# Kernel tuning notes

Measured on AMD Instinct MI355X. Metric: run time of the kernel, lower is better.

Reference implementation:

```python
import jax, jax.numpy as jnp
import numpy as np

N = 100000
E = 1600000
F_IN = 128
HID = 128
CLS = 40


def setup_inputs() -> dict:
    key = jax.random.key(0)
    ks = jax.random.split(key, 8)
    x = jax.random.normal(ks[0], (N, F_IN), dtype=jnp.float32)
    edge_index = jax.random.randint(ks[1], (2, E), 0, N, dtype=jnp.int64)
    s1 = 1.0 / np.sqrt(F_IN)
    s2 = 1.0 / np.sqrt(HID)
    return {
        "x": x,
        "edge_index": edge_index,
        "Wl1": jax.random.uniform(ks[2], (F_IN, HID), jnp.float32, -s1, s1),
        "Wr1": jax.random.uniform(ks[3], (F_IN, HID), jnp.float32, -s1, s1),
        "b1": jnp.zeros((HID,), jnp.float32),
        "Wl2": jax.random.uniform(ks[4], (HID, CLS), jnp.float32, -s2, s2),
        "Wr2": jax.random.uniform(ks[5], (HID, CLS), jnp.float32, -s2, s2),
        "b2": jnp.zeros((CLS,), jnp.float32),
    }


def _sage_conv(x, src, dst, Wl, Wr, b):
    # mean aggregation of neighbor features: messages flow src -> dst
    msg = x[src]                                                  # [E, F]
    agg = jax.ops.segment_sum(msg, dst, num_segments=N)          # [N, F]
    deg = jax.ops.segment_sum(jnp.ones((src.shape[0],), x.dtype), dst,
                              num_segments=N)                     # [N]
    mean = agg / jnp.maximum(deg, 1.0)[:, None]
    # PyG SAGEConv: lin_l(aggregated) + lin_r(root); bias on lin_l only
    return mean @ Wl + x @ Wr + b


def reference(x, edge_index, Wl1, Wr1, b1, Wl2, Wr2, b2):
    src, dst = edge_index[0], edge_index[1]
    h = _sage_conv(x, src, dst, Wl1, Wr1, b1)
    h = jax.nn.relu(h)
    # dropout is identity in eval mode
    out = _sage_conv(h, src, dst, Wl2, Wr2, b2)
    return out
```

## Files before the change

kernel.cpp:

```cpp
#include <hip/hip_runtime.h>

#define F 128
#define CLSN 40
#define NFINE_MAX 256
#define PCAP 10240
#define TILE 4096
#define STAGE_CAP 10240
#define QSCALE 22.0f

typedef __attribute__((ext_vector_type(8))) short short8v;
typedef __attribute__((ext_vector_type(4))) float float4v;

static __device__ inline ushort f2bf(float f) {
  uint u = __float_as_uint(f);
  uint r = (u + 0x7FFFu + ((u >> 16) & 1u)) >> 16;
  return (ushort)r;
}
static __device__ inline float bfLo(uint u) { return __uint_as_float(u << 16); }
static __device__ inline float bfHi(uint u) { return __uint_as_float(u & 0xFFFF0000u); }
static __device__ inline int sb(uint v, int sh) { return (int)(signed char)(v >> sh); }
static __device__ inline unsigned char q8(float f) {
  float t = rintf(f * QSCALE);
  t = fminf(fmaxf(t, -127.f), 127.f);
  return (unsigned char)(signed char)(int)t;
}
static __device__ inline unsigned char q8s(float f, float qs) {
  float t = rintf(f * qs);
  t = fminf(fmaxf(t, -127.f), 127.f);
  return (unsigned char)(signed char)(int)t;
}

__global__ __launch_bounds__(256) void k_prep(const float* __restrict__ x,
                                              ushort* __restrict__ xb,
                                              unsigned char* __restrict__ xq,
                                              const float* __restrict__ Wl1,
                                              const float* __restrict__ Wr1,
                                              ushort* __restrict__ Wp1,
                                              const float* __restrict__ Wl2,
                                              const float* __restrict__ Wr2,
                                              ushort* __restrict__ Wpl,
                                              ushort* __restrict__ Wpr,
                                              int* __restrict__ fcur,
                                              int nelem4, int castBlocks, int nfine) {
  const int blk = blockIdx.x;
  if (blk < castBlocks) {
    int i = blk * 256 + threadIdx.x;
    if (i < nelem4) {
      float4 v = reinterpret_cast<const float4*>(x)[i];
      ushort4 o;
      o.x = f2bf(v.x); o.y = f2bf(v.y); o.z = f2bf(v.z); o.w = f2bf(v.w);
      reinterpret_cast<ushort4*>(xb)[i] = o;
      uchar4 q;
      q.x = q8(v.x); q.y = q8(v.y); q.z = q8(v.z); q.w = q8(v.w);
      reinterpret_cast<uchar4*>(xq)[i] = q;
    }
  } else if (blk < castBlocks + 16) {
    int t = (blk - castBlocks) * 256 + threadIdx.x;
    int lane = t & 63, f = (t >> 6) & 7, ks = t >> 9;
    int col = f * 16 + (lane & 15);
    int k0 = ks * 32 + (lane >> 4) * 8;
#pragma unroll
    for (int j = 0; j < 8; ++j) {
      int k = k0 + j;
      float w = (k < 128) ? Wl1[k * 128 + col] : Wr1[(k - 128) * 128 + col];
      Wp1[t * 8 + j] = f2bf(w);
    }
  } else if (blk < castBlocks + 22) {
    int t = (blk - castBlocks - 16) * 256 + threadIdx.x;
    const float* W = (t < 768) ? Wl2 : Wr2;
    ushort* Wp = (t < 768) ? Wpl : Wpr;
    int tt = (t < 768) ? t : t - 768;
    int lane = tt & 63, rem = tt >> 6;
    int f = rem % 3, ks = rem / 3;
    int col = f * 16 + (lane & 15);
    int k0 = ks * 32 + (lane >> 4) * 8;
#pragma unroll
    for (int j = 0; j < 8; ++j) {
      int k = k0 + j;
      float w = (col < CLSN) ? W[k * CLSN + col] : 0.f;
      Wp[tt * 8 + j] = f2bf(w);
    }
  } else {
    int i = threadIdx.x;
    if (i < nfine) fcur[i] = i * PCAP;
  }
}

__global__ __launch_bounds__(256) void k_partition(const int* __restrict__ src,
                                                   const int* __restrict__ dst,
                                                   int* __restrict__ fcur,
                                                   uint* __restrict__ pairs, int E) {
  __shared__ int hh[NFINE_MAX];
  __shared__ int bb[NFINE_MAX];
  __shared__ unsigned char ebkt[TILE];
  __shared__ ushort dlow[TILE];
  const int tid = threadIdx.x;
  const int tile0 = blockIdx.x * TILE;
  const int lim = min(TILE, E - tile0);
  for (int i = tid; i < NFINE_MAX; i += 256) hh[i] = 0;
  __syncthreads();
  for (int i = tid; i < lim; i += 256) {
    int d = dst[tile0 + i];
    int b = d >> 9;
    ebkt[i] = (unsigned char)b;
    dlow[i] = (ushort)(d & 511);
    atomicAdd(&hh[b], 1);
  }
  __syncthreads();
  for (int i = tid; i < NFINE_MAX; i += 256) {
    int c = hh[i];
    bb[i] = c ? atomicAdd(&fcur[i], c) : 0;
    hh[i] = 0;
  }
  __syncthreads();
  for (int i = tid; i < lim; i += 256) {
    int b = ebkt[i];
    int r = atomicAdd(&hh[b], 1);
    uint p = (uint)src[tile0 + i] | ((uint)dlow[i] << 17);
    pairs[bb[b] + r] = p;
  }
}

__global__ __launch_bounds__(256) void k_local_scatter(const uint* __restrict__ pairs,
                                                       const int* __restrict__ fcur,
                                                       int* __restrict__ offsets,
                                                       int* __restrict__ srcs,
                                                       int n, int E, int nfine) {
  __shared__ int s_cnt[512];
  __shared__ int s_scan[512];
  __shared__ int s_stage[STAGE_CAP];
  const int b = blockIdx.x, tid = threadIdx.x;
  const int node0 = b << 9;
  const int pbase = b * PCAP;
  int c_i = (tid < nfine) ? (fcur[tid] - tid * PCAP) : 0;
  s_scan[tid] = c_i;
  __syncthreads();
  for (int d = 1; d < 256; d <<= 1) {
    int u = (tid >= d) ? s_scan[tid - d] : 0;
    __syncthreads();
    s_scan[tid] += u;
    __syncthreads();
  }
  const int ecnt = fcur[b] - pbase;
  const int ebase = s_scan[b] - ecnt;
  __syncthreads();
  s_cnt[tid] = 0;
  s_cnt[tid + 256] = 0;
  __syncthreads();
  for (int i = tid; i < ecnt; i += 256) atomicAdd(&s_cnt[pairs[pbase + i] >> 17], 1);
  __syncthreads();
  s_scan[tid] = s_cnt[tid];
  s_scan[tid + 256] = s_cnt[tid + 256];
  __syncthreads();
  for (int d = 1; d < 512; d <<= 1) {
    int v0 = (tid >= d) ? s_scan[tid - d] : 0;
    int v1 = (tid + 256 >= d) ? s_scan[tid + 256 - d] : 0;
    __syncthreads();
    s_scan[tid] += v0;
    s_scan[tid + 256] += v1;
    __syncthreads();
  }
  int e0 = s_scan[tid] - s_cnt[tid];
  int e1 = s_scan[tid + 256] - s_cnt[tid + 256];
  if (node0 + tid < n) offsets[node0 + tid] = ebase + e0;
  if (node0 + tid + 256 < n) offsets[node0 + tid + 256] = ebase + e1;
  if (b == gridDim.x - 1 && tid == 0) offsets[n] = E;
  __syncthreads();
  s_cnt[tid] = e0;
  s_cnt[tid + 256] = e1;
  __syncthreads();
  for (int i = tid; i < ecnt; i += 256) {
    uint p = pairs[pbase + i];
    int v = (int)(p >> 17);
    int s = (int)(p & 0x1FFFFu);
    int pos = atomicAdd(&s_cnt[v], 1);
    if (pos < STAGE_CAP) s_stage[pos] = s;
    else srcs[ebase + pos] = s;
  }
  __syncthreads();
  int lim = min(ecnt, STAGE_CAP);
  for (int i = tid; i < lim; i += 256) srcs[ebase + i] = s_stage[i];
}

__global__ __launch_bounds__(256) void k_agg_x(const unsigned char* __restrict__ xq,
                                               const int* __restrict__ offsets,
                                               const int* __restrict__ srcs,
                                               ushort* __restrict__ mean, int n) {
  const int wid = (blockIdx.x * 256 + threadIdx.x) >> 6;
  const int lane = threadIdx.x & 63;
  const int g = lane >> 4, cl = lane & 15;
  const int node = wid * 4 + g;
  if (node >= n) return;
  const uint2* fp = reinterpret_cast<const uint2*>(xq);
  const int beg = offsets[node];
  const int deg = offsets[node + 1] - beg;
  int s0 = 0, s1 = 0, s2 = 0, s3 = 0, s4 = 0, s5 = 0, s6 = 0, s7 = 0;
  for (int chunk = 0; chunk < deg; chunk += 16) {
    int cnt = min(16, deg - chunk);
    int s = (cl < cnt) ? srcs[beg + chunk + cl] : 0;
    int k = 0;
    for (; k + 7 < cnt; k += 8) {
      int r0 = __shfl(s, g * 16 + k);
      int r1 = __shfl(s, g * 16 + k + 1);
      int r2 = __shfl(s, g * 16 + k + 2);
      int r3 = __shfl(s, g * 16 + k + 3);
      int r4 = __shfl(s, g * 16 + k + 4);
      int r5 = __shfl(s, g * 16 + k + 5);
      int r6 = __shfl(s, g * 16 + k + 6);
      int r7 = __shfl(s, g * 16 + k + 7);
      uint2 v0 = fp[(size_t)r0 * 16 + cl];
      uint2 v1 = fp[(size_t)r1 * 16 + cl];
      uint2 v2 = fp[(size_t)r2 * 16 + cl];
      uint2 v3 = fp[(size_t)r3 * 16 + cl];
      uint2 v4 = fp[(size_t)r4 * 16 + cl];
      uint2 v5 = fp[(size_t)r5 * 16 + cl];
      uint2 v6 = fp[(size_t)r6 * 16 + cl];
      uint2 v7 = fp[(size_t)r7 * 16 + cl];
      s0 += sb(v0.x, 0) + sb(v1.x, 0) + sb(v2.x, 0) + sb(v3.x, 0) +
            sb(v4.x, 0) + sb(v5.x, 0) + sb(v6.x, 0) + sb(v7.x, 0);
      s1 += sb(v0.x, 8) + sb(v1.x, 8) + sb(v2.x, 8) + sb(v3.x, 8) +
            sb(v4.x, 8) + sb(v5.x, 8) + sb(v6.x, 8) + sb(v7.x, 8);
      s2 += sb(v0.x, 16) + sb(v1.x, 16) + sb(v2.x, 16) + sb(v3.x, 16) +
            sb(v4.x, 16) + sb(v5.x, 16) + sb(v6.x, 16) + sb(v7.x, 16);
      s3 += sb(v0.x, 24) + sb(v1.x, 24) + sb(v2.x, 24) + sb(v3.x, 24) +
            sb(v4.x, 24) + sb(v5.x, 24) + sb(v6.x, 24) + sb(v7.x, 24);
      s4 += sb(v0.y, 0) + sb(v1.y, 0) + sb(v2.y, 0) + sb(v3.y, 0) +
            sb(v4.y, 0) + sb(v5.y, 0) + sb(v6.y, 0) + sb(v7.y, 0);
      s5 += sb(v0.y, 8) + sb(v1.y, 8) + sb(v2.y, 8) + sb(v3.y, 8) +
            sb(v4.y, 8) + sb(v5.y, 8) + sb(v6.y, 8) + sb(v7.y, 8);
      s6 += sb(v0.y, 16) + sb(v1.y, 16) + sb(v2.y, 16) + sb(v3.y, 16) +
            sb(v4.y, 16) + sb(v5.y, 16) + sb(v6.y, 16) + sb(v7.y, 16);
      s7 += sb(v0.y, 24) + sb(v1.y, 24) + sb(v2.y, 24) + sb(v3.y, 24) +
            sb(v4.y, 24) + sb(v5.y, 24) + sb(v6.y, 24) + sb(v7.y, 24);
    }
    for (; k < cnt; ++k) {
      int r0 = __shfl(s, g * 16 + k);
      uint2 v0 = fp[(size_t)r0 * 16 + cl];
      s0 += sb(v0.x, 0); s1 += sb(v0.x, 8);
      s2 += sb(v0.x, 16); s3 += sb(v0.x, 24);
      s4 += sb(v0.y, 0); s5 += sb(v0.y, 8);
      s6 += sb(v0.y, 16); s7 += sb(v0.y, 24);
    }
  }
  float inv = deg > 0 ? 1.f / (QSCALE * (float)deg) : 0.f;
  uint4 o;
  o.x = (uint)f2bf((float)s0 * inv) | ((uint)f2bf((float)s1 * inv) << 16);
  o.y = (uint)f2bf((float)s2 * inv) | ((uint)f2bf((float)s3 * inv) << 16);
  o.z = (uint)f2bf((float)s4 * inv) | ((uint)f2bf((float)s5 * inv) << 16);
  o.w = (uint)f2bf((float)s6 * inv) | ((uint)f2bf((float)s7 * inv) << 16);
  reinterpret_cast<uint4*>(mean)[(size_t)node * 16 + cl] = o;
}

__global__ __launch_bounds__(256) void k_scl(const float* __restrict__ bmax,
                                             float* __restrict__ scl, int nb) {
  __shared__ float s_w[4];
  float mx = 0.f;
  for (int i = threadIdx.x; i < nb; i += 256) mx = fmaxf(mx, bmax[i]);
#pragma unroll
  for (int d = 32; d; d >>= 1) mx = fmaxf(mx, __shfl_xor(mx, d));
  if ((threadIdx.x & 63) == 0) s_w[threadIdx.x >> 6] = mx;
  __syncthreads();
  if (threadIdx.x == 0)
    *scl = fmaxf(fmaxf(s_w[0], s_w[1]), fmaxf(s_w[2], s_w[3]));
}

__global__ __launch_bounds__(256) void k_quant_p(const ushort* __restrict__ p,
                                                 const float* __restrict__ scl,
                                                 unsigned char* __restrict__ pq, int nelem4) {
  int i = blockIdx.x * 256 + threadIdx.x;
  if (i >= nelem4) return;
  float ma = *scl;
  float qs = ma > 0.f ? 127.f / ma : 0.f;
  uint2 v = reinterpret_cast<const uint2*>(p)[i];
  uchar4 q;
  q.x = q8s(bfLo(v.x), qs);
  q.y = q8s(bfHi(v.x), qs);
  q.z = q8s(bfLo(v.y), qs);
  q.w = q8s(bfHi(v.y), qs);
  reinterpret_cast<uchar4*>(pq)[i] = q;
}

__global__ __launch_bounds__(256) void k_agg_p(const unsigned char* __restrict__ pq,
                                               const int* __restrict__ offsets,
                                               const int* __restrict__ srcs,
                                               const float* __restrict__ scl,
                                               float* __restrict__ m, int n) {
  const int wid = (blockIdx.x * 256 + threadIdx.x) >> 6;
  const int lane = threadIdx.x & 63;
  const int g = lane >> 3, cl = lane & 7;
  const int node = wid * 8 + g;
  if (node >= n) return;
  const uint2* pp = reinterpret_cast<const uint2*>(pq);
  const int beg = offsets[node];
  const int deg = offsets[node + 1] - beg;
  int s0 = 0, s1 = 0, s2 = 0, s3 = 0, s4 = 0, s5 = 0, s6 = 0, s7 = 0;
  for (int chunk = 0; chunk < deg; chunk += 8) {
    int cnt = min(8, deg - chunk);
    int s = (cl < cnt) ? srcs[beg + chunk + cl] : 0;
    int k = 0;
    for (; k + 7 < cnt; k += 8) {
      int r0 = __shfl(s, g * 8 + k);
      int r1 = __shfl(s, g * 8 + k + 1);
      int r2 = __shfl(s, g * 8 + k + 2);
      int r3 = __shfl(s, g * 8 + k + 3);
      int r4 = __shfl(s, g * 8 + k + 4);
      int r5 = __shfl(s, g * 8 + k + 5);
      int r6 = __shfl(s, g * 8 + k + 6);
      int r7 = __shfl(s, g * 8 + k + 7);
      uint2 v0 = pp[(size_t)r0 * 8 + cl];
      uint2 v1 = pp[(size_t)r1 * 8 + cl];
      uint2 v2 = pp[(size_t)r2 * 8 + cl];
      uint2 v3 = pp[(size_t)r3 * 8 + cl];
      uint2 v4 = pp[(size_t)r4 * 8 + cl];
      uint2 v5 = pp[(size_t)r5 * 8 + cl];
      uint2 v6 = pp[(size_t)r6 * 8 + cl];
      uint2 v7 = pp[(size_t)r7 * 8 + cl];
      s0 += sb(v0.x, 0) + sb(v1.x, 0) + sb(v2.x, 0) + sb(v3.x, 0) +
            sb(v4.x, 0) + sb(v5.x, 0) + sb(v6.x, 0) + sb(v7.x, 0);
      s1 += sb(v0.x, 8) + sb(v1.x, 8) + sb(v2.x, 8) + sb(v3.x, 8) +
            sb(v4.x, 8) + sb(v5.x, 8) + sb(v6.x, 8) + sb(v7.x, 8);
      s2 += sb(v0.x, 16) + sb(v1.x, 16) + sb(v2.x, 16) + sb(v3.x, 16) +
            sb(v4.x, 16) + sb(v5.x, 16) + sb(v6.x, 16) + sb(v7.x, 16);
      s3 += sb(v0.x, 24) + sb(v1.x, 24) + sb(v2.x, 24) + sb(v3.x, 24) +
            sb(v4.x, 24) + sb(v5.x, 24) + sb(v6.x, 24) + sb(v7.x, 24);
      s4 += sb(v0.y, 0) + sb(v1.y, 0) + sb(v2.y, 0) + sb(v3.y, 0) +
            sb(v4.y, 0) + sb(v5.y, 0) + sb(v6.y, 0) + sb(v7.y, 0);
      s5 += sb(v0.y, 8) + sb(v1.y, 8) + sb(v2.y, 8) + sb(v3.y, 8) +
            sb(v4.y, 8) + sb(v5.y, 8) + sb(v6.y, 8) + sb(v7.y, 8);
      s6 += sb(v0.y, 16) + sb(v1.y, 16) + sb(v2.y, 16) + sb(v3.y, 16) +
            sb(v4.y, 16) + sb(v5.y, 16) + sb(v6.y, 16) + sb(v7.y, 16);
      s7 += sb(v0.y, 24) + sb(v1.y, 24) + sb(v2.y, 24) + sb(v3.y, 24) +
            sb(v4.y, 24) + sb(v5.y, 24) + sb(v6.y, 24) + sb(v7.y, 24);
    }
    for (; k < cnt; ++k) {
      int r0 = __shfl(s, g * 8 + k);
      uint2 v0 = pp[(size_t)r0 * 8 + cl];
      s0 += sb(v0.x, 0); s1 += sb(v0.x, 8);
      s2 += sb(v0.x, 16); s3 += sb(v0.x, 24);
      s4 += sb(v0.y, 0); s5 += sb(v0.y, 8);
      s6 += sb(v0.y, 16); s7 += sb(v0.y, 24);
    }
  }
  float ma = *scl;
  float inv = deg > 0 ? ma / (127.f * (float)deg) : 0.f;
  float4* mp = reinterpret_cast<float4*>(m);
  mp[(size_t)node * 16 + cl * 2] =
      make_float4((float)s0 * inv, (float)s1 * inv, (float)s2 * inv, (float)s3 * inv);
  mp[(size_t)node * 16 + cl * 2 + 1] =
      make_float4((float)s4 * inv, (float)s5 * inv, (float)s6 * inv, (float)s7 * inv);
}

__global__ __launch_bounds__(256) void k_mfma1(const ushort* __restrict__ meanb,
                                               const ushort* __restrict__ rootb,
                                               const ushort* __restrict__ Wp,
                                               const float* __restrict__ b,
                                               ushort* __restrict__ h, int nrows) {
  __shared__ __align__(16) ushort As[64 * 256];
  const int tid = threadIdx.x;
  const int row0 = blockIdx.x * 64;
#pragma unroll
  for (int i = 0; i < 8; ++i) {
    int c = tid + i * 256;
    int r = c >> 5;
    int c16 = c & 31;
    int grow = row0 + r;
    short8v v = {0, 0, 0, 0, 0, 0, 0, 0};
    if (grow < nrows) {
      const ushort* srcp = (c16 < 16) ? (meanb + (size_t)grow * 128 + c16 * 8)
                                      : (rootb + (size_t)grow * 128 + (c16 - 16) * 8);
      v = *reinterpret_cast<const short8v*>(srcp);
    }
    int dbyte = r * 512 + ((c16 * 16) ^ ((r & 7) << 4));
    *reinterpret_cast<short8v*>(reinterpret_cast<char*>(As) + dbyte) = v;
  }
  __syncthreads();
  const int lane = tid & 63;
  const int rbase = (tid >> 6) * 16;
  const int arow = rbase + (lane & 15);
  const int axor = (arow & 7) << 4;
  const short8v* Wp8 = reinterpret_cast<const short8v*>(Wp);
  float4v acc[8];
#pragma unroll
  for (int f = 0; f < 8; ++f) acc[f] = {0.f, 0.f, 0.f, 0.f};
#pragma unroll
  for (int ks = 0; ks < 8; ++ks) {
    int abyte = arow * 512 + ((ks * 64 + (lane >> 4) * 16) ^ axor);
    short8v a = *reinterpret_cast<const short8v*>(reinterpret_cast<const char*>(As) + abyte);
#pragma unroll
    for (int f = 0; f < 8; ++f) {
      short8v bf = Wp8[(ks * 8 + f) * 64 + lane];
      acc[f] = __builtin_amdgcn_mfma_f32_16x16x32_bf16(a, bf, acc[f], 0, 0, 0);
    }
  }
  const int col_lo = lane & 15;
  const int rq = (lane >> 4) * 4;
#pragma unroll
  for (int f = 0; f < 8; ++f) {
    int col = f * 16 + col_lo;
    float bias = b[col];
#pragma unroll
    for (int r = 0; r < 4; ++r) {
      int row = row0 + rbase + rq + r;
      if (row < nrows) {
        float vv = fmaxf(acc[f][r] + bias, 0.f);
        h[(size_t)row * 128 + col] = f2bf(vv);
      }
    }
  }
}

__global__ __launch_bounds__(256) void k_proj2(const ushort* __restrict__ hb,
                                               const ushort* __restrict__ Wp,
                                               ushort* __restrict__ p,
                                               float* __restrict__ bmax, int nrows) {
  __shared__ __align__(16) ushort As[64 * 128];
  __shared__ float s_wmax[4];
  const int tid = threadIdx.x;
  const int row0 = blockIdx.x * 64;
#pragma unroll
  for (int i = 0; i < 4; ++i) {
    int c = tid + i * 256;
    int r = c >> 4;
    int c16 = c & 15;
    int grow = row0 + r;
    short8v v = {0, 0, 0, 0, 0, 0, 0, 0};
    if (grow < nrows) v = *reinterpret_cast<const short8v*>(hb + (size_t)grow * 128 + c16 * 8);
    int dbyte = r * 256 + ((c16 * 16) ^ ((r & 7) << 4));
    *reinterpret_cast<short8v*>(reinterpret_cast<char*>(As) + dbyte) = v;
  }
  __syncthreads();
  const int lane = tid & 63;
  const int rbase = (tid >> 6) * 16;
  const int arow = rbase + (lane & 15);
  const int axor = (arow & 7) << 4;
  const short8v* Wp8 = reinterpret_cast<const short8v*>(Wp);
  float4v acc[3];
#pragma unroll
  for (int f = 0; f < 3; ++f) acc[f] = {0.f, 0.f, 0.f, 0.f};
#pragma unroll
  for (int ks = 0; ks < 4; ++ks) {
    int abyte = arow * 256 + ((ks * 64 + (lane >> 4) * 16) ^ axor);
    short8v a = *reinterpret_cast<const short8v*>(reinterpret_cast<const char*>(As) + abyte);
#pragma unroll
    for (int f = 0; f < 3; ++f) {
      short8v bf = Wp8[(ks * 3 + f) * 64 + lane];
      acc[f] = __builtin_amdgcn_mfma_f32_16x16x32_bf16(a, bf, acc[f], 0, 0, 0);
    }
  }
  const int col_lo = lane & 15;
  const int rq = (lane >> 4) * 4;
  float mx = 0.f;
#pragma unroll
  for (int f = 0; f < 3; ++f) {
    int col = f * 16 + col_lo;
#pragma unroll
    for (int r = 0; r < 4; ++r) {
      int row = row0 + rbase + rq + r;
      if (row < nrows) {
        p[(size_t)row * 64 + col] = f2bf(acc[f][r]);
        mx = fmaxf(mx, fabsf(acc[f][r]));
      }
    }
  }
#pragma unroll
  for (int r = 0; r < 4; ++r) {
    int row = row0 + rbase + rq + r;
    if (row < nrows) p[(size_t)row * 64 + 48 + col_lo] = 0;
  }
#pragma unroll
  for (int d = 32; d; d >>= 1) mx = fmaxf(mx, __shfl_xor(mx, d));
  if (lane == 0) s_wmax[tid >> 6] = mx;
  __syncthreads();
  if (tid == 0)
    bmax[blockIdx.x] = fmaxf(fmaxf(s_wmax[0], s_wmax[1]), fmaxf(s_wmax[2], s_wmax[3]));
}

__global__ __launch_bounds__(256) void k_root2(const ushort* __restrict__ hb,
                                               const ushort* __restrict__ Wp,
                                               const float* __restrict__ b,
                                               const float* __restrict__ m,
                                               float* __restrict__ out, int nrows) {
  __shared__ __align__(16) ushort As[64 * 128];
  const int tid = threadIdx.x;
  const int row0 = blockIdx.x * 64;
#pragma unroll
  for (int i = 0; i < 4; ++i) {
    int c = tid + i * 256;
    int r = c >> 4;
    int c16 = c & 15;
    int grow = row0 + r;
    short8v v = {0, 0, 0, 0, 0, 0, 0, 0};
    if (grow < nrows) v = *reinterpret_cast<const short8v*>(hb + (size_t)grow * 128 + c16 * 8);
    int dbyte = r * 256 + ((c16 * 16) ^ ((r & 7) << 4));
    *reinterpret_cast<short8v*>(reinterpret_cast<char*>(As) + dbyte) = v;
  }
  __syncthreads();
  const int lane = tid & 63;
  const int rbase = (tid >> 6) * 16;
  const int arow = rbase + (lane & 15);
  const int axor = (arow & 7) << 4;
  const short8v* Wp8 = reinterpret_cast<const short8v*>(Wp);
  float4v acc[3];
#pragma unroll
  for (int f = 0; f < 3; ++f) acc[f] = {0.f, 0.f, 0.f, 0.f};
#pragma unroll
  for (int ks = 0; ks < 4; ++ks) {
    int abyte = arow * 256 + ((ks * 64 + (lane >> 4) * 16) ^ axor);
    short8v a = *reinterpret_cast<const short8v*>(reinterpret_cast<const char*>(As) + abyte);
#pragma unroll
    for (int f = 0; f < 3; ++f) {
      short8v bf = Wp8[(ks * 3 + f) * 64 + lane];
      acc[f] = __builtin_amdgcn_mfma_f32_16x16x32_bf16(a, bf, acc[f], 0, 0, 0);
    }
  }
  const int col_lo = lane & 15;
  const int rq = (lane >> 4) * 4;
#pragma unroll
  for (int f = 0; f < 3; ++f) {
    int col = f * 16 + col_lo;
    if (col < CLSN) {
      float bias = b[col];
#pragma unroll
      for (int r = 0; r < 4; ++r) {
        int row = row0 + rbase + rq + r;
        if (row < nrows)
          out[(size_t)row * CLSN + col] = acc[f][r] + bias + m[(size_t)row * 64 + col];
      }
    }
  }
}

extern "C" void kernel_launch(void* const* d_in, const int* in_sizes, int n_in,
                              void* d_out, int out_size, void* d_ws, size_t ws_size,
                              hipStream_t stream) {
  const float* x = (const float*)d_in[0];
  const int* ei = (const int*)d_in[1];
  const float* Wl1 = (const float*)d_in[2];
  const float* Wr1 = (const float*)d_in[3];
  const float* b1 = (const float*)d_in[4];
  const float* Wl2 = (const float*)d_in[5];
  const float* Wr2 = (const float*)d_in[6];
  const float* b2 = (const float*)d_in[7];
  float* out = (float*)d_out;

  const int n = in_sizes[0] / F;
  const int E = in_sizes[1] / 2;
  const int* src = ei;
  const int* dst = ei + E;

  const int nfine = (n + 511) >> 9;
  const int ngemm = (n + 63) / 64;

  size_t off = 0;
  auto alloc = [&](size_t bytes) {
    size_t cur = off;
    off = (off + bytes + 255) & ~(size_t)255;
    return cur;
  };
  char* w = (char*)d_ws;
  int* offsets = (int*)(w + alloc((size_t)(n + 1) * 4));
  int* srcs = (int*)(w + alloc((size_t)E * 4));
  int* fcur = (int*)(w + alloc(NFINE_MAX * 4));
  float* scl = (float*)(w + alloc(256));
  float* bmax = (float*)(w + alloc((size_t)(ngemm + 8) * 4));
  ushort* xb = (ushort*)(w + alloc((size_t)n * F * 2));
  ushort* hb = (ushort*)(w + alloc((size_t)n * F * 2));
  ushort* meanb = (ushort*)(w + alloc((size_t)n * F * 2));
  ushort* Wp1 = (ushort*)(w + alloc(32768 * 2));
  ushort* Wp2l = (ushort*)(w + alloc(6144 * 2));
  ushort* Wp2r = (ushort*)(w + alloc(6144 * 2));
  (void)ws_size;
  uint* pairs = (uint*)meanb;
  ushort* p64 = meanb;
  unsigned char* pq8 = (unsigned char*)(meanb + (size_t)n * 64);
  float* m64 = (float*)xb;
  unsigned char* xq8 = (unsigned char*)hb;

  const int castBlocks = (n * 32 + 255) / 256;

  k_prep<<<castBlocks + 23, 256, 0, stream>>>(x, xb, xq8, Wl1, Wr1, Wp1, Wl2, Wr2,
                                              Wp2l, Wp2r, fcur, n * 32, castBlocks,
                                              nfine);

  k_partition<<<(E + TILE - 1) / TILE, 256, 0, stream>>>(src, dst, fcur, pairs, E);
  k_local_scatter<<<nfine, 256, 0, stream>>>(pairs, fcur, offsets, srcs, n, E, nfine);

  k_agg_x<<<(n + 15) / 16, 256, 0, stream>>>(xq8, offsets, srcs, meanb, n);
  k_mfma1<<<ngemm, 256, 0, stream>>>(meanb, xb, Wp1, b1, hb, n);

  k_proj2<<<ngemm, 256, 0, stream>>>(hb, Wp2l, p64, bmax, n);
  k_scl<<<1, 256, 0, stream>>>(bmax, scl, ngemm);
  k_quant_p<<<(n * 16 + 255) / 256, 256, 0, stream>>>(p64, scl, pq8, n * 16);
  k_agg_p<<<(n + 31) / 32, 256, 0, stream>>>(pq8, offsets, srcs, scl, m64, n);
  k_root2<<<ngemm, 256, 0, stream>>>(hb, Wp2r, b2, m64, out, n);
}
```

Baseline: 196.9 us.

## Fuse layer-1 GEMM with layer-2 projection and aggregation with root GEMM

Merges k_mfma1 and k_proj2 so the layer-1 output tile stays in LDS and is projected by Wl2 immediately. The global max is now computed by the last-arriving block through an atomic ticket counter, which replaces the separate k_scl launch. k_agg_p and k_root2 are merged so the aggregated mean is kept in LDS rather than written to and reread from a float buffer. This removes three launches and one fp32 intermediate round trip. The cost is higher LDS use per block, which may lower occupancy in the gather-heavy fused kernel, plus the threadfence and atomic serialization.

After: 254.8 us. 1.29x slower.

```diff
diff --git a/kernel.cpp b/kernel.cpp
--- a/kernel.cpp
+++ b/kernel.cpp
@@ -41,6 +41,7 @@
                                               ushort* __restrict__ Wpl,
                                               ushort* __restrict__ Wpr,
                                               int* __restrict__ fcur,
+                                              int* __restrict__ counter,
                                               int nelem4, int castBlocks, int nfine) {
   const int blk = blockIdx.x;
   if (blk < castBlocks) {
@@ -83,6 +84,7 @@
   } else {
     int i = threadIdx.x;
     if (i < nfine) fcur[i] = i * PCAP;
+    if (i == 0) *counter = 0;
   }
 }
 
@@ -251,17 +253,127 @@
   reinterpret_cast<uint4*>(mean)[(size_t)node * 16 + cl] = o;
 }
 
-__global__ __launch_bounds__(256) void k_scl(const float* __restrict__ bmax,
-                                             float* __restrict__ scl, int nb) {
-  __shared__ float s_w[4];
+__global__ __launch_bounds__(256) void k_mfma1p(const ushort* __restrict__ meanb,
+                                                const ushort* __restrict__ rootb,
+                                                const ushort* __restrict__ Wp,
+                                                const float* __restrict__ b,
+                                                const ushort* __restrict__ Wp2,
+                                                ushort* __restrict__ h,
+                                                ushort* __restrict__ p,
+                                                float* __restrict__ bmax,
+                                                int* __restrict__ counter,
+                                                float* __restrict__ scl, int nrows) {
+  __shared__ __align__(16) ushort As[64 * 256];
+  __shared__ float s_wmax[4];
+  __shared__ int s_last;
+  const int tid = threadIdx.x;
+  const int row0 = blockIdx.x * 64;
+#pragma unroll
+  for (int i = 0; i < 8; ++i) {
+    int c = tid + i * 256;
+    int r = c >> 5;
+    int c16 = c & 31;
+    int grow = row0 + r;
+    short8v v = {0, 0, 0, 0, 0, 0, 0, 0};
+    if (grow < nrows) {
+      const ushort* srcp = (c16 < 16) ? (meanb + (size_t)grow * 128 + c16 * 8)
+                                      : (rootb + (size_t)grow * 128 + (c16 - 16) * 8);
+      v = *reinterpret_cast<const short8v*>(srcp);
+    }
+    int dbyte = r * 512 + ((c16 * 16) ^ ((r & 7) << 4));
+    *reinterpret_cast<short8v*>(reinterpret_cast<char*>(As) + dbyte) = v;
+  }
+  __syncthreads();
+  const int lane = tid & 63;
+  const int rbase = (tid >> 6) * 16;
+  const int arow = rbase + (lane & 15);
+  const int axor = (arow & 7) << 4;
+  const short8v* Wp8 = reinterpret_cast<const short8v*>(Wp);
+  float4v acc[8];
+#pragma unroll
+  for (int f = 0; f < 8; ++f) acc[f] = {0.f, 0.f, 0.f, 0.f};
+#pragma unroll
+  for (int ks = 0; ks < 8; ++ks) {
+    int abyte = arow * 512 + ((ks * 64 + (lane >> 4) * 16) ^ axor);
+    short8v a = *reinterpret_cast<const short8v*>(reinterpret_cast<const char*>(As) + abyte);
+#pragma unroll
+    for (int f = 0; f < 8; ++f) {
+      short8v bf = Wp8[(ks * 8 + f) * 64 + lane];
+      acc[f] = __builtin_amdgcn_mfma_f32_16x16x32_bf16(a, bf, acc[f], 0, 0, 0);
+    }
+  }
+  const int col_lo = lane & 15;
+  const int rq = (lane >> 4) * 4;
+  __syncthreads();
+#pragma unroll
+  for (int f = 0; f < 8; ++f) {
+    int col = f * 16 + col_lo;
+    float bias = b[col];
+#pragma unroll
+    for (int r = 0; r < 4; ++r) {
+      int row = row0 + rbase + rq + r;
+      ushort hv = f2bf(fmaxf(acc[f][r] + bias, 0.f));
+      if (row < nrows) h[(size_t)row * 128 + col] = hv;
+      int lrow = rbase + rq + r;
+      int lbyte = lrow * 256 + (((col >> 3) * 16) ^ ((lrow & 7) << 4)) + (col & 7) * 2;
+      *reinterpret_cast<ushort*>(reinterpret_cast<char*>(As) + lbyte) = hv;
+    }
+  }
+  __syncthreads();
+  const short8v* Wq8 = reinterpret_cast<const short8v*>(Wp2);
+  float4v acc2[3];
+#pragma unroll
+  for (int f = 0; f < 3; ++f) acc2[f] = {0.f, 0.f, 0.f, 0.f};
+#pragma unroll
+  for (int ks = 0; ks < 4; ++ks) {
+    int abyte = arow * 256 + ((ks * 64 + (lane >> 4) * 16) ^ axor);
+    short8v a = *reinterpret_cast<const short8v*>(reinterpret_cast<const char*>(As) + abyte);
+#pragma unroll
+    for (int f = 0; f < 3; ++f) {
+      short8v bf = Wq8[(ks * 3 + f) * 64 + lane];
+      acc2[f] = __builtin_amdgcn_mfma_f32_16x16x32_bf16(a, bf, acc2[f], 0, 0, 0);
+    }
+  }
   float mx = 0.f;
-  for (int i = threadIdx.x; i < nb; i += 256) mx = fmaxf(mx, bmax[i]);
+#pragma unroll
+  for (int f = 0; f < 3; ++f) {
+    int col = f * 16 + col_lo;
+#pragma unroll
+    for (int r = 0; r < 4; ++r) {
+      int row = row0 + rbase + rq + r;
+      if (row < nrows) {
+        p[(size_t)row * 64 + col] = f2bf(acc2[f][r]);
+        mx = fmaxf(mx, fabsf(acc2[f][r]));
+      }
+    }
+  }
+#pragma unroll
+  for (int r = 0; r < 4; ++r) {
+    int row = row0 + rbase + rq + r;
+    if (row < nrows) p[(size_t)row * 64 + 48 + col_lo] = 0;
+  }
 #pragma unroll
   for (int d = 32; d; d >>= 1) mx = fmaxf(mx, __shfl_xor(mx, d));
-  if ((threadIdx.x & 63) == 0) s_w[threadIdx.x >> 6] = mx;
-  __syncthreads();
-  if (threadIdx.x == 0)
-    *scl = fmaxf(fmaxf(s_w[0], s_w[1]), fmaxf(s_w[2], s_w[3]));
+  if (lane == 0) s_wmax[tid >> 6] = mx;
+  __syncthreads();
+  if (tid == 0) {
+    bmax[blockIdx.x] = fmaxf(fmaxf(s_wmax[0], s_wmax[1]), fmaxf(s_wmax[2], s_wmax[3]));
+    __threadfence();
+    int ticket = atomicAdd(counter, 1);
+    s_last = (ticket == (int)gridDim.x - 1) ? 1 : 0;
+  }
+  __syncthreads();
+  if (s_last) {
+    __threadfence();
+    float m2 = 0.f;
+    for (int i = tid; i < (int)gridDim.x; i += 256) m2 = fmaxf(m2, bmax[i]);
+#pragma unroll
+    for (int d = 32; d; d >>= 1) m2 = fmaxf(m2, __shfl_xor(m2, d));
+    if ((tid & 63) == 0) s_wmax[tid >> 6] = m2;
+    __syncthreads();
+    if (tid == 0)
+      *scl = fmaxf(fmaxf(s_wmax[0], s_wmax[1]), fmaxf(s_wmax[2], s_wmax[3]));
+  }
 }
 
 __global__ __launch_bounds__(256) void k_quant_p(const ushort* __restrict__ p,
@@ -280,143 +392,91 @@
   reinterpret_cast<uchar4*>(pq)[i] = q;
 }
 
-__global__ __launch_bounds__(256) void k_agg_p(const unsigned char* __restrict__ pq,
-                                               const int* __restrict__ offsets,
-                                               const int* __restrict__ srcs,
-                                               const float* __restrict__ scl,
-                                               float* __restrict__ m, int n) {
-  const int wid = (blockIdx.x * 256 + threadIdx.x) >> 6;
-  const int lane = threadIdx.x & 63;
-  const int g = lane >> 3, cl = lane & 7;
-  const int node = wid * 8 + g;
-  if (node >= n) return;
-  const uint2* pp = reinterpret_cast<const uint2*>(pq);
-  const int beg = offsets[node];
-  const int deg = offsets[node + 1] - beg;
-  int s0 = 0, s1 = 0, s2 = 0, s3 = 0, s4 = 0, s5 = 0, s6 = 0, s7 = 0;
-  for (int chunk = 0; chunk < deg; chunk += 8) {
-    int cnt = min(8, deg - chunk);
-    int s = (cl < cnt) ? srcs[beg + chunk + cl] : 0;
-    int k = 0;
-    for (; k + 7 < cnt; k += 8) {
-      int r0 = __shfl(s, g * 8 + k);
-      int r1 = __shfl(s, g * 8 + k + 1);
-      int r2 = __shfl(s, g * 8 + k + 2);
-      int r3 = __shfl(s, g * 8 + k + 3);
-      int r4 = __shfl(s, g * 8 + k + 4);
-      int r5 = __shfl(s, g * 8 + k + 5);
-      int r6 = __shfl(s, g * 8 + k + 6);
-      int r7 = __shfl(s, g * 8 + k + 7);
-      uint2 v0 = pp[(size_t)r0 * 8 + cl];
-      uint2 v1 = pp[(size_t)r1 * 8 + cl];
-      uint2 v2 = pp[(size_t)r2 * 8 + cl];
-      uint2 v3 = pp[(size_t)r3 * 8 + cl];
-      uint2 v4 = pp[(size_t)r4 * 8 + cl];
-      uint2 v5 = pp[(size_t)r5 * 8 + cl];
-      uint2 v6 = pp[(size_t)r6 * 8 + cl];
-      uint2 v7 = pp[(size_t)r7 * 8 + cl];
-      s0 += sb(v0.x, 0) + sb(v1.x, 0) + sb(v2.x, 0) + sb(v3.x, 0) +
-            sb(v4.x, 0) + sb(v5.x, 0) + sb(v6.x, 0) + sb(v7.x, 0);
-      s1 += sb(v0.x, 8) + sb(v1.x, 8) + sb(v2.x, 8) + sb(v3.x, 8) +
-            sb(v4.x, 8) + sb(v5.x, 8) + sb(v6.x, 8) + sb(v7.x, 8);
-      s2 += sb(v0.x, 16) + sb(v1.x, 16) + sb(v2.x, 16) + sb(v3.x, 16) +
-            sb(v4.x, 16) + sb(v5.x, 16) + sb(v6.x, 16) + sb(v7.x, 16);
-      s3 += sb(v0.x, 24) + sb(v1.x, 24) + sb(v2.x, 24) + sb(v3.x, 24) +
-            sb(v4.x, 24) + sb(v5.x, 24) + sb(v6.x, 24) + sb(v7.x, 24);
-      s4 += sb(v0.y, 0) + sb(v1.y, 0) + sb(v2.y, 0) + sb(v3.y, 0) +
-            sb(v4.y, 0) + sb(v5.y, 0) + sb(v6.y, 0) + sb(v7.y, 0);
-      s5 += sb(v0.y, 8) + sb(v1.y, 8) + sb(v2.y, 8) + sb(v3.y, 8) +
-            sb(v4.y, 8) + sb(v5.y, 8) + sb(v6.y, 8) + sb(v7.y, 8);
-      s6 += sb(v0.y, 16) + sb(v1.y, 16) + sb(v2.y, 16) + sb(v3.y, 16) +
-            sb(v4.y, 16) + sb(v5.y, 16) + sb(v6.y, 16) + sb(v7.y, 16);
-      s7 += sb(v0.y, 24) + sb(v1.y, 24) + sb(v2.y, 24) + sb(v3.y, 24) +
-            sb(v4.y, 24) + sb(v5.y, 24) + sb(v6.y, 24) + sb(v7.y, 24);
-    }
-    for (; k < cnt; ++k) {
-      int r0 = __shfl(s, g * 8 + k);
-      uint2 v0 = pp[(size_t)r0 * 8 + cl];
-      s0 += sb(v0.x, 0); s1 += sb(v0.x, 8);
-      s2 += sb(v0.x, 16); s3 += sb(v0.x, 24);
-      s4 += sb(v0.y, 0); s5 += sb(v0.y, 8);
-      s6 += sb(v0.y, 16); s7 += sb(v0.y, 24);
-    }
-  }
-  float ma = *scl;
-  float inv = deg > 0 ? ma / (127.f * (float)deg) : 0.f;
-  float4* mp = reinterpret_cast<float4*>(m);
-  mp[(size_t)node * 16 + cl * 2] =
-      make_float4((float)s0 * inv, (float)s1 * inv, (float)s2 * inv, (float)s3 * inv);
-  mp[(size_t)node * 16 + cl * 2 + 1] =
-      make_float4((float)s4 * inv, (float)s5 * inv, (float)s6 * inv, (float)s7 * inv);
-}
-
-__global__ __launch_bounds__(256) void k_mfma1(const ushort* __restrict__ meanb,
-                                               const ushort* __restrict__ rootb,
-                                               const ushort* __restrict__ Wp,
-                                               const float* __restrict__ b,
-                                               ushort* __restrict__ h, int nrows) {
-  __shared__ __align__(16) ushort As[64 * 256];
+__global__ __launch_bounds__(256) void k_aggroot2(const unsigned char* __restrict__ pq,
+                                                  const int* __restrict__ offsets,
+                                                  const int* __restrict__ srcs,
+                                                  const float* __restrict__ scl,
+                                                  const ushort* __restrict__ hb,
+                                                  const ushort* __restrict__ Wp,
+                                                  const float* __restrict__ b,
+                                                  float* __restrict__ out, int nrows) {
+  __shared__ __align__(16) ushort As[64 * 128];
+  __shared__ float m_lds[64][64];
   const int tid = threadIdx.x;
   const int row0 = blockIdx.x * 64;
-#pragma unroll
-  for (int i = 0; i < 8; ++i) {
-    int c = tid + i * 256;
-    int r = c >> 5;
-    int c16 = c & 31;
-    int grow = row0 + r;
-    short8v v = {0, 0, 0, 0, 0, 0, 0, 0};
-    if (grow < nrows) {
-      const ushort* srcp = (c16 < 16) ? (meanb + (size_t)grow * 128 + c16 * 8)
-                                      : (rootb + (size_t)grow * 128 + (c16 - 16) * 8);
-      v = *reinterpret_cast<const short8v*>(srcp);
-    }
-    int dbyte = r * 512 + ((c16 * 16) ^ ((r & 7) << 4));
-    *reinterpret_cast<short8v*>(reinterpret_cast<char*>(As) + dbyte) = v;
-  }
-  __syncthreads();
   const int lane = tid & 63;
-  const int rbase = (tid >> 6) * 16;
-  const int arow = rbase + (lane & 15);
-  const int axor = (arow & 7) << 4;
-  const short8v* Wp8 = reinterpret_cast<const short8v*>(Wp);
-  float4v acc[8];
-#pragma unroll
-  for (int f = 0; f < 8; ++f) acc[f] = {0.f, 0.f, 0.f, 0.f};
-#pragma unroll
-  for (int ks = 0; ks < 8; ++ks) {
-    int abyte = arow * 512 + ((ks * 64 + (lane >> 4) * 16) ^ axor);
-    short8v a = *reinterpret_cast<const short8v*>(reinterpret_cast<const char*>(As) + abyte);
-#pragma unroll
-    for (int f = 0; f < 8; ++f) {
-      short8v bf = Wp8[(ks * 8 + f) * 64 + lane];
-      acc[f] = __builtin_amdgcn_mfma_f32_16x16x32_bf16(a, bf, acc[f], 0, 0, 0);
-    }
-  }
-  const int col_lo = lane & 15;
-  const int rq = (lane >> 4) * 4;
-#pragma unroll
-  for (int f = 0; f < 8; ++f) {
-    int col = f * 16 + col_lo;
-    float bias = b[col];
-#pragma unroll
-    for (int r = 0; r < 4; ++r) {
-      int row = row0 + rbase + rq + r;
-      if (row < nrows) {
-        float vv = fmaxf(acc[f][r] + bias, 0.f);
-        h[(size_t)row * 128 + col] = f2bf(vv);
+  const int wv = tid >> 6;
+  {
+    const int g = lane >> 3, cl = lane & 7;
+    const uint2* pp = reinterpret_cast<const uint2*>(pq);
+    const float ma = *scl;
+#pragma unroll
+    for (int it = 0; it < 2; ++it) {
+      const int node = row0 + it * 32 + wv * 8 + g;
+      if (node < nrows) {
+        const int beg = offsets[node];
+        const int deg = offsets[node + 1] - beg;
+        int s0 = 0, s1 = 0, s2 = 0, s3 = 0, s4 = 0, s5 = 0, s6 = 0, s7 = 0;
+        for (int chunk = 0; chunk < deg; chunk += 8) {
+          int cnt = min(8, deg - chunk);
+          int s = (cl < cnt) ? srcs[beg + chunk + cl] : 0;
+          int k = 0;
+          for (; k + 7 < cnt; k += 8) {
+            int r0 = __shfl(s, g * 8 + k);
+            int r1 = __shfl(s, g * 8 + k + 1);
+            int r2 = __shfl(s, g * 8 + k + 2);
+            int r3 = __shfl(s, g * 8 + k + 3);
+            int r4 = __shfl(s, g * 8 + k + 4);
+            int r5 = __shfl(s, g * 8 + k + 5);
+            int r6 = __shfl(s, g * 8 + k + 6);
+            int r7 = __shfl(s, g * 8 + k + 7);
+            uint2 v0 = pp[(size_t)r0 * 8 + cl];
+            uint2 v1 = pp[(size_t)r1 * 8 + cl];
+            uint2 v2 = pp[(size_t)r2 * 8 + cl];
+            uint2 v3 = pp[(size_t)r3 * 8 + cl];
+            uint2 v4 = pp[(size_t)r4 * 8 + cl];
+            uint2 v5 = pp[(size_t)r5 * 8 + cl];
+            uint2 v6 = pp[(size_t)r6 * 8 + cl];
+            uint2 v7 = pp[(size_t)r7 * 8 + cl];
+            s0 += sb(v0.x, 0) + sb(v1.x, 0) + sb(v2.x, 0) + sb(v3.x, 0) +
+                  sb(v4.x, 0) + sb(v5.x, 0) + sb(v6.x, 0) + sb(v7.x, 0);
+            s1 += sb(v0.x, 8) + sb(v1.x, 8) + sb(v2.x, 8) + sb(v3.x, 8) +
+                  sb(v4.x, 8) + sb(v5.x, 8) + sb(v6.x, 8) + sb(v7.x, 8);
+            s2 += sb(v0.x, 16) + sb(v1.x, 16) + sb(v2.x, 16) + sb(v3.x, 16) +
+                  sb(v4.x, 16) + sb(v5.x, 16) + sb(v6.x, 16) + sb(v7.x, 16);
+            s3 += sb(v0.x, 24) + sb(v1.x, 24) + sb(v2.x, 24) + sb(v3.x, 24) +
+                  sb(v4.x, 24) + sb(v5.x, 24) + sb(v6.x, 24) + sb(v7.x, 24);
+            s4 += sb(v0.y, 0) + sb(v1.y, 0) + sb(v2.y, 0) + sb(v3.y, 0) +
+                  sb(v4.y, 0) + sb(v5.y, 0) + sb(v6.y, 0) + sb(v7.y, 0);
+            s5 += sb(v0.y, 8) + sb(v1.y, 8) + sb(v2.y, 8) + sb(v3.y, 8) +
+                  sb(v4.y, 8) + sb(v5.y, 8) + sb(v6.y, 8) + sb(v7.y, 8);
+            s6 += sb(v0.y, 16) + sb(v1.y, 16) + sb(v2.y, 16) + sb(v3.y, 16) +
+                  sb(v4.y, 16) + sb(v5.y, 16) + sb(v6.y, 16) + sb(v7.y, 16);
+            s7 += sb(v0.y, 24) + sb(v1.y, 24) + sb(v2.y, 24) + sb(v3.y, 24) +
+                  sb(v4.y, 24) + sb(v5.y, 24) + sb(v6.y, 24) + sb(v7.y, 24);
+          }
+          for (; k < cnt; ++k) {
+            int r0 = __shfl(s, g * 8 + k);
+            uint2 v0 = pp[(size_t)r0 * 8 + cl];
+            s0 += sb(v0.x, 0); s1 += sb(v0.x, 8);
+            s2 += sb(v0.x, 16); s3 += sb(v0.x, 24);
+            s4 += sb(v0.y, 0); s5 += sb(v0.y, 8);
+            s6 += sb(v0.y, 16); s7 += sb(v0.y, 24);
+          }
+        }
+        float inv = deg > 0 ? ma / (127.f * (float)deg) : 0.f;
+        int ln = node - row0;
+        m_lds[ln][cl * 8 + 0] = (float)s0 * inv;
+        m_lds[ln][cl * 8 + 1] = (float)s1 * inv;
+        m_lds[ln][cl * 8 + 2] = (float)s2 * inv;
+        m_lds[ln][cl * 8 + 3] = (float)s3 * inv;
+        m_lds[ln][cl * 8 + 4] = (float)s4 * inv;
+        m_lds[ln][cl * 8 + 5] = (float)s5 * inv;
+        m_lds[ln][cl * 8 + 6] = (float)s6 * inv;
+        m_lds[ln][cl * 8 + 7] = (float)s7 * inv;
       }
     }
   }
-}
-
-__global__ __launch_bounds__(256) void k_proj2(const ushort* __restrict__ hb,
-                                               const ushort* __restrict__ Wp,
-                                               ushort* __restrict__ p,
-                                               float* __restrict__ bmax, int nrows) {
-  __shared__ __align__(16) ushort As[64 * 128];
-  __shared__ float s_wmax[4];
-  const int tid = threadIdx.x;
-  const int row0 = blockIdx.x * 64;
 #pragma unroll
   for (int i = 0; i < 4; ++i) {
     int c = tid + i * 256;
@@ -429,8 +489,7 @@
     *reinterpret_cast<short8v*>(reinterpret_cast<char*>(As) + dbyte) = v;
   }
   __syncthreads();
-  const int lane = tid & 63;
-  const int rbase = (tid >> 6) * 16;
+  const int rbase = wv * 16;
   const int arow = rbase + (lane & 15);
   const int axor = (arow & 7) << 4;
   const short8v* Wp8 = reinterpret_cast<const short8v*>(Wp);
@@ -449,72 +508,6 @@
   }
   const int col_lo = lane & 15;
   const int rq = (lane >> 4) * 4;
-  float mx = 0.f;
-#pragma unroll
-  for (int f = 0; f < 3; ++f) {
-    int col = f * 16 + col_lo;
-#pragma unroll
-    for (int r = 0; r < 4; ++r) {
-      int row = row0 + rbase + rq + r;
-      if (row < nrows) {
-        p[(size_t)row * 64 + col] = f2bf(acc[f][r]);
-        mx = fmaxf(mx, fabsf(acc[f][r]));
-      }
-    }
-  }
-#pragma unroll
-  for (int r = 0; r < 4; ++r) {
-    int row = row0 + rbase + rq + r;
-    if (row < nrows) p[(size_t)row * 64 + 48 + col_lo] = 0;
-  }
-#pragma unroll
-  for (int d = 32; d; d >>= 1) mx = fmaxf(mx, __shfl_xor(mx, d));
-  if (lane == 0) s_wmax[tid >> 6] = mx;
-  __syncthreads();
-  if (tid == 0)
-    bmax[blockIdx.x] = fmaxf(fmaxf(s_wmax[0], s_wmax[1]), fmaxf(s_wmax[2], s_wmax[3]));
-}
-
-__global__ __launch_bounds__(256) void k_root2(const ushort* __restrict__ hb,
-                                               const ushort* __restrict__ Wp,
-                                               const float* __restrict__ b,
-                                               const float* __restrict__ m,
-                                               float* __restrict__ out, int nrows) {
-  __shared__ __align__(16) ushort As[64 * 128];
-  const int tid = threadIdx.x;
-  const int row0 = blockIdx.x * 64;
-#pragma unroll
-  for (int i = 0; i < 4; ++i) {
-    int c = tid + i * 256;
-    int r = c >> 4;
-    int c16 = c & 15;
-    int grow = row0 + r;
-    short8v v = {0, 0, 0, 0, 0, 0, 0, 0};
-    if (grow < nrows) v = *reinterpret_cast<const short8v*>(hb + (size_t)grow * 128 + c16 * 8);
-    int dbyte = r * 256 + ((c16 * 16) ^ ((r & 7) << 4));
-    *reinterpret_cast<short8v*>(reinterpret_cast<char*>(As) + dbyte) = v;
-  }
-  __syncthreads();
-  const int lane = tid & 63;
-  const int rbase = (tid >> 6) * 16;
-  const int arow = rbase + (lane & 15);
-  const int axor = (arow & 7) << 4;
-  const short8v* Wp8 = reinterpret_cast<const short8v*>(Wp);
-  float4v acc[3];
-#pragma unroll
-  for (int f = 0; f < 3; ++f) acc[f] = {0.f, 0.f, 0.f, 0.f};
-#pragma unroll
-  for (int ks = 0; ks < 4; ++ks) {
-    int abyte = arow * 256 + ((ks * 64 + (lane >> 4) * 16) ^ axor);
-    short8v a = *reinterpret_cast<const short8v*>(reinterpret_cast<const char*>(As) + abyte);
-#pragma unroll
-    for (int f = 0; f < 3; ++f) {
-      short8v bf = Wp8[(ks * 3 + f) * 64 + lane];
-      acc[f] = __builtin_amdgcn_mfma_f32_16x16x32_bf16(a, bf, acc[f], 0, 0, 0);
-    }
-  }
-  const int col_lo = lane & 15;
-  const int rq = (lane >> 4) * 4;
 #pragma unroll
   for (int f = 0; f < 3; ++f) {
     int col = f * 16 + col_lo;
@@ -524,7 +517,8 @@
       for (int r = 0; r < 4; ++r) {
         int row = row0 + rbase + rq + r;
         if (row < nrows)
-          out[(size_t)row * CLSN + col] = acc[f][r] + bias + m[(size_t)row * 64 + col];
+          out[(size_t)row * CLSN + col] =
+              acc[f][r] + bias + m_lds[rbase + rq + r][col];
       }
     }
   }
@@ -562,6 +556,7 @@
   int* srcs = (int*)(w + alloc((size_t)E * 4));
   int* fcur = (int*)(w + alloc(NFINE_MAX * 4));
   float* scl = (float*)(w + alloc(256));
+  int* counter = (int*)(w + alloc(256));
   float* bmax = (float*)(w + alloc((size_t)(ngemm + 8) * 4));
   ushort* xb = (ushort*)(w + alloc((size_t)n * F * 2));
   ushort* hb = (ushort*)(w + alloc((size_t)n * F * 2));
@@ -573,24 +568,21 @@
   uint* pairs = (uint*)meanb;
   ushort* p64 = meanb;
   unsigned char* pq8 = (unsigned char*)(meanb + (size_t)n * 64);
-  float* m64 = (float*)xb;
   unsigned char* xq8 = (unsigned char*)hb;
 
   const int castBlocks = (n * 32 + 255) / 256;
 
   k_prep<<<castBlocks + 23, 256, 0, stream>>>(x, xb, xq8, Wl1, Wr1, Wp1, Wl2, Wr2,
-                                              Wp2l, Wp2r, fcur, n * 32, castBlocks,
-                                              nfine);
+                                              Wp2l, Wp2r, fcur, counter, n * 32,
+                                              castBlocks, nfine);
 
   k_partition<<<(E + TILE - 1) / TILE, 256, 0, stream>>>(src, dst, fcur, pairs, E);
   k_local_scatter<<<nfine, 256, 0, stream>>>(pairs, fcur, offsets, srcs, n, E, nfine);
 
   k_agg_x<<<(n + 15) / 16, 256, 0, stream>>>(xq8, offsets, srcs, meanb, n);
-  k_mfma1<<<ngemm, 256, 0, stream>>>(meanb, xb, Wp1, b1, hb, n);
-
-  k_proj2<<<ngemm, 256, 0, stream>>>(hb, Wp2l, p64, bmax, n);
-  k_scl<<<1, 256, 0, stream>>>(bmax, scl, ngemm);
+  k_mfma1p<<<ngemm, 256, 0, stream>>>(meanb, xb, Wp1, b1, Wp2l, hb, p64, bmax,
+                                      counter, scl, n);
+
   k_quant_p<<<(n * 16 + 255) / 256, 256, 0, stream>>>(p64, scl, pq8, n * 16);
-  k_agg_p<<<(n + 31) / 32, 256, 0, stream>>>(pq8, offsets, srcs, scl, m64, n);
-  k_root2<<<ngemm, 256, 0, stream>>>(hb, Wp2r, b2, m64, out, n);
-}
+  k_aggroot2<<<ngemm, 256, 0, stream>>>(pq8, offsets, srcs, scl, hb, Wp2r, b2, out, n);
+}
```
